# Performance work log

Measured on AMD Instinct MI355X. Metric: run time of the kernel, lower is better.

Reference implementation:

```python
import jax, jax.numpy as jnp
import numpy as np

D_MODEL = 1024
N_HEAD = 16
POWER = 4
EPS = 1e-6
MASK_FILL = -1000.0


def setup_inputs() -> dict:
    key = jax.random.key(0)
    ks = jax.random.split(key, 10)
    B, T, C = 2, 2048, D_MODEL
    sc = 1.0 / np.sqrt(C)
    inp = {
        "x": jax.random.normal(ks[0], (B, T, C), jnp.float32),
        "Wq": jax.random.normal(ks[1], (C, C), jnp.float32) * sc,
        "bq": jnp.zeros((C,), jnp.float32),
        "Wk": jax.random.normal(ks[2], (C, C), jnp.float32) * sc,
        "bk": jnp.zeros((C,), jnp.float32),
        "Wv": jax.random.normal(ks[3], (C, C), jnp.float32) * sc,
        "bv": jnp.zeros((C,), jnp.float32),
        "Wo": jax.random.normal(ks[4], (C, C), jnp.float32) * sc,
        "bo": jnp.zeros((C,), jnp.float32),
        "score_gain": jnp.asarray(4.0, jnp.float32),
        # True above the diagonal -> masked (causal)
        "causal_mask": jnp.triu(jnp.ones((T, T), jnp.bool_), k=1),
    }
    return inp


def rational_softmax(x):
    s = x / (jnp.abs(x) + 1.0)          # squash to (-1, 1)
    p = ((s + 1.0) * 0.5) ** POWER      # (0,1) then sharpen
    return p / (jnp.sum(p, axis=-1, keepdims=True) + EPS)


def reference(x, Wq, bq, Wk, bk, Wv, bv, Wo, bo, score_gain, causal_mask):
    B, T, C = x.shape
    H, D = N_HEAD, C // N_HEAD
    q = (x @ Wq + bq).reshape(B, T, H, D)
    k = (x @ Wk + bk).reshape(B, T, H, D)
    v = (x @ Wv + bv).reshape(B, T, H, D)
    # scores: (B, H, T, T)
    scores = jnp.einsum('bqhd,bkhd->bhqk', q, k)
    scores = scores - jnp.mean(scores, axis=-1, keepdims=True)
    mad = jnp.mean(jnp.abs(scores), axis=-1, keepdims=True) + 1e-6
    scores = scores / mad * score_gain
    scores = jnp.where(causal_mask, MASK_FILL, scores)
    attn = rational_softmax(scores)
    out = jnp.einsum('bhqk,bkhd->bqhd', attn, v).reshape(B, T, C)
    return out @ Wo + bo
```

## Files before the change

### kernel.cpp

```cpp
#include <hip/hip_runtime.h>
#include <hip/hip_bf16.h>
#include <cstdint>

#define BDIM 2
#define TSEQ 2048
#define CDIM 1024
#define NH 16
#define HD 64
#define NTOK (BDIM*TSEQ)
#define MASK_FILL_V (-1000.0f)
#define EPS_V (1e-6f)

typedef short bf16x8 __attribute__((ext_vector_type(8)));
typedef float f32x4  __attribute__((ext_vector_type(4)));

__device__ __forceinline__ float bf2f(unsigned short u) {
    union { unsigned int i; float f; } x; x.i = ((unsigned int)u) << 16; return x.f;
}
__device__ __forceinline__ unsigned short f2bf(float v) {
    __hip_bfloat16 h = __float2bfloat16(v);
    union { __hip_bfloat16 h; unsigned short u; } c; c.h = h; return c.u;
}
__device__ __forceinline__ float unpk_lo(unsigned int u) {
    union { unsigned int i; float f; } x; x.i = u << 16; return x.f;
}
__device__ __forceinline__ float unpk_hi(unsigned int u) {
    union { unsigned int i; float f; } x; x.i = u & 0xFFFF0000u; return x.f;
}
__device__ __forceinline__ unsigned int pk2(float lo, float hi) {
    unsigned int r;
    asm("v_cvt_pk_bf16_f32 %0, %1, %2" : "=v"(r) : "v"(lo), "v"(hi));
    return r;
}

__device__ __forceinline__ bool dt_is_bf16(const void* gain_p) {
    return ((*(const unsigned int*)gain_p) & 0xFFFFu) == 0x4080u;
}
__device__ __forceinline__ float ld1(const void* p, size_t i, bool bf) {
    return bf ? bf2f(((const unsigned short*)p)[i]) : ((const float*)p)[i];
}

__device__ __forceinline__ void gl2lds16(const unsigned short* g, unsigned short* l) {
    __builtin_amdgcn_global_load_lds(
        (const __attribute__((address_space(1))) unsigned int*)g,
        (__attribute__((address_space(3))) unsigned int*)l, 16, 0, 0);
}

__global__ __launch_bounds__(256) void pack_x_kernel(
    const void* __restrict__ X, const void* __restrict__ gain_p,
    unsigned short* __restrict__ Xb)
{
    const bool bf = dt_is_bf16(gain_p);
    size_t i = ((size_t)blockIdx.x * 256 + threadIdx.x) * 8;
    if (bf) {
        *(bf16x8*)&Xb[i] = *(const bf16x8*)((const unsigned short*)X + i);
    } else {
        const float* xf = (const float*)X;
        float4 a = *(const float4*)&xf[i];
        float4 b = *(const float4*)&xf[i + 4];
        bf16x8 o;
        o[0]=(short)f2bf(a.x); o[1]=(short)f2bf(a.y); o[2]=(short)f2bf(a.z); o[3]=(short)f2bf(a.w);
        o[4]=(short)f2bf(b.x); o[5]=(short)f2bf(b.y); o[6]=(short)f2bf(b.z); o[7]=(short)f2bf(b.w);
        *(bf16x8*)&Xb[i] = o;
    }
}

__global__ __launch_bounds__(256) void pack_wt_kernel(
    const void* __restrict__ Wq, const void* __restrict__ Wk,
    const void* __restrict__ Wv, const void* __restrict__ Wo,
    const void* __restrict__ gain_p, unsigned short* __restrict__ Wt)
{
    __shared__ __align__(16) unsigned short tile[64][72];
    const bool bf = dt_is_bf16(gain_p);
    const int which = blockIdx.z;
    const void* W = (which == 0) ? Wq : (which == 1) ? Wk : (which == 2) ? Wv : Wo;
    const int k0 = blockIdx.y * 64, n0 = blockIdx.x * 64;
    const int t = threadIdx.x;
    const int r = t >> 2, cb = (t & 3) * 16;
    if (bf) {
        const unsigned short* wsd = (const unsigned short*)W;
        *(bf16x8*)&tile[r][cb]     = *(const bf16x8*)&wsd[(size_t)(k0 + r) * CDIM + n0 + cb];
        *(bf16x8*)&tile[r][cb + 8] = *(const bf16x8*)&wsd[(size_t)(k0 + r) * CDIM + n0 + cb + 8];
    } else {
        const float* wf = (const float*)W;
        const float* src = &wf[(size_t)(k0 + r) * CDIM + n0 + cb];
        float4 f0 = *(const float4*)&src[0];
        float4 f1 = *(const float4*)&src[4];
        float4 f2 = *(const float4*)&src[8];
        float4 f3 = *(const float4*)&src[12];
        bf16x8 o0, o1;
        o0[0]=(short)f2bf(f0.x); o0[1]=(short)f2bf(f0.y); o0[2]=(short)f2bf(f0.z); o0[3]=(short)f2bf(f0.w);
        o0[4]=(short)f2bf(f1.x); o0[5]=(short)f2bf(f1.y); o0[6]=(short)f2bf(f1.z); o0[7]=(short)f2bf(f1.w);
        o1[0]=(short)f2bf(f2.x); o1[1]=(short)f2bf(f2.y); o1[2]=(short)f2bf(f2.z); o1[3]=(short)f2bf(f2.w);
        o1[4]=(short)f2bf(f3.x); o1[5]=(short)f2bf(f3.y); o1[6]=(short)f2bf(f3.z); o1[7]=(short)f2bf(f3.w);
        *(bf16x8*)&tile[r][cb]     = o0;
        *(bf16x8*)&tile[r][cb + 8] = o1;
    }
    __syncthreads();
    const int dr = t >> 2, tb = (t & 3) * 16;
    __align__(16) unsigned short tmp[16];
#pragma unroll
    for (int j = 0; j < 16; ++j) tmp[j] = tile[tb + j][dr];
    unsigned short* dst = Wt + ((size_t)(which * CDIM + n0 + dr)) * CDIM + k0 + tb;
    *(bf16x8*)&dst[0] = *(bf16x8*)&tmp[0];
    *(bf16x8*)&dst[8] = *(bf16x8*)&tmp[8];
}

__global__ __launch_bounds__(256) void gemm_mfma_kernel(
    const unsigned short* __restrict__ A,
    const unsigned short* __restrict__ Bt,
    const void* __restrict__ b0p, const void* __restrict__ b1p,
    const void* __restrict__ b2p,
    const void* __restrict__ gain_p,
    unsigned short* __restrict__ qkv,
    void* __restrict__ outp, int mode)
{
    __shared__ __align__(16) unsigned short As[128 * 32];
    __shared__ __align__(16) unsigned short Bs[128 * 32];

    const bool bf = dt_is_bf16(gain_p);
    const int t = threadIdx.x;
    const int w = t >> 6, lane = t & 63, quad = lane >> 4, l16 = lane & 15;
    const int wm = w >> 1, wn = w & 1;

    const int gx = gridDim.x, gy = gridDim.y;
    const int lin = blockIdx.y * gx + blockIdx.x;
    const int chunk = (gx * gy) >> 3;
    const int nid = (lin & 7) * chunk + (lin >> 3);
    const int n0 = (nid / gy) * 128, m0 = (nid % gy) * 128;

    const unsigned short* Ag = A  + (size_t)m0 * CDIM;
    const unsigned short* Bg = Bt + (size_t)n0 * CDIM;

    f32x4 acc[4][4];
#pragma unroll
    for (int mt = 0; mt < 4; ++mt)
#pragma unroll
        for (int nt = 0; nt < 4; ++nt)
            acc[mt][nt] = (f32x4){0.f, 0.f, 0.f, 0.f};

    for (int kt = 0; kt < CDIM / 32; ++kt) {
        const int k0 = kt * 32;
#pragma unroll
        for (int i = 0; i < 2; ++i) {
            const int chunkid = (i * 4 + w) * 64 + lane;
            const int row = chunkid >> 2, kp = (chunkid & 3) * 8;
            gl2lds16(Ag + (size_t)row * CDIM + k0 + kp, &As[(i * 4 + w) * 512]);
            gl2lds16(Bg + (size_t)row * CDIM + k0 + kp, &Bs[(i * 4 + w) * 512]);
        }
        __syncthreads();
        bf16x8 af[4], bfr[4];
#pragma unroll
        for (int mt = 0; mt < 4; ++mt)
            af[mt] = *(const bf16x8*)&As[(wm * 64 + mt * 16 + l16) * 32 + quad * 8];
#pragma unroll
        for (int nt = 0; nt < 4; ++nt)
            bfr[nt] = *(const bf16x8*)&Bs[(wn * 64 + nt * 16 + l16) * 32 + quad * 8];
#pragma unroll
        for (int mt = 0; mt < 4; ++mt)
#pragma unroll
            for (int nt = 0; nt < 4; ++nt)
                acc[mt][nt] = __builtin_amdgcn_mfma_f32_16x16x32_bf16(af[mt], bfr[nt], acc[mt][nt], 0, 0, 0);
        __syncthreads();
    }

    if (mode == 0) {
        const int which = n0 >> 10;
        if (which < 2) {
            const void* biasP = (which == 0) ? b0p : b1p;
            unsigned short* out = qkv + (size_t)which * NTOK * CDIM;
#pragma unroll
            for (int nt = 0; nt < 4; ++nt) {
                const int np = (n0 & 1023) + wn * 64 + nt * 16 + l16;
                const int h = np >> 6, d = np & 63;
                const float bias = ld1(biasP, np, bf);
#pragma unroll
                for (int mt = 0; mt < 4; ++mt)
#pragma unroll
                    for (int r = 0; r < 4; ++r) {
                        const int m = m0 + wm * 64 + mt * 16 + quad * 4 + r;
                        const int bb = m >> 11, tt = m & (TSEQ - 1);
                        out[(((size_t)(bb * NH + h)) * TSEQ + tt) * HD + d] =
                            f2bf(acc[mt][nt][r] + bias);
                    }
            }
        } else {
            unsigned short* vt = (unsigned short*)outp;
#pragma unroll
            for (int nt = 0; nt < 4; ++nt) {
                const int np = (n0 & 1023) + wn * 64 + nt * 16 + l16;
                const int h = np >> 6, d = np & 63;
                const float bias = ld1(b2p, np, bf);
#pragma unroll
                for (int mt = 0; mt < 4; ++mt) {
                    const int m = m0 + wm * 64 + mt * 16 + quad * 4;
                    const int bb = m >> 11, tt0 = m & (TSEQ - 1);
                    unsigned int lo = ((unsigned int)f2bf(acc[mt][nt][1] + bias) << 16)
                                    |  (unsigned int)f2bf(acc[mt][nt][0] + bias);
                    unsigned int hi = ((unsigned int)f2bf(acc[mt][nt][3] + bias) << 16)
                                    |  (unsigned int)f2bf(acc[mt][nt][2] + bias);
                    uint2 pk; pk.x = lo; pk.y = hi;
                    *(uint2*)&vt[((size_t)(bb * NH + h) * HD + d) * TSEQ + tt0] = pk;
                }
            }
        }
    } else {
#pragma unroll
        for (int nt = 0; nt < 4; ++nt) {
            const int np = n0 + wn * 64 + nt * 16 + l16;
            const float bias = ld1(b0p, np, bf);
#pragma unroll
            for (int mt = 0; mt < 4; ++mt)
#pragma unroll
                for (int r = 0; r < 4; ++r) {
                    const int m = m0 + wm * 64 + mt * 16 + quad * 4 + r;
                    const float v = acc[mt][nt][r] + bias;
                    if (bf) ((__hip_bfloat16*)outp)[(size_t)m * CDIM + np] = __float2bfloat16(v);
                    else    ((float*)outp)[(size_t)m * CDIM + np] = v;
                }
        }
    }
}

__global__ __launch_bounds__(256) void ksum_kernel(
    const unsigned short* __restrict__ Kb, float* __restrict__ Ksum)
{
    __shared__ float red[32][64];
    const int bh = blockIdx.x;
    const int t = threadIdx.x;
    const int d8 = (t & 7) * 8, g = t >> 3;
    const unsigned short* kp = Kb + (size_t)bh * TSEQ * HD;
    float s[8] = {};
    for (int tt = g; tt < TSEQ; tt += 32) {
        bf16x8 v = *(const bf16x8*)&kp[(size_t)tt * HD + d8];
#pragma unroll
        for (int j = 0; j < 8; ++j) s[j] += bf2f((unsigned short)v[j]);
    }
#pragma unroll
    for (int j = 0; j < 8; ++j) red[g][d8 + j] = s[j];
    __syncthreads();
    if (t < 64) {
        float tot = 0.f;
#pragma unroll
        for (int gg = 0; gg < 32; ++gg) tot += red[gg][t];
        Ksum[(size_t)bh * HD + t] = tot;
    }
}

#define QROWS 16
#define NQT (TSEQ / QROWS)

__global__ __launch_bounds__(512, 2) void attn_mfma_kernel(
    const unsigned short* __restrict__ Qb,
    const unsigned short* __restrict__ Kb,
    const unsigned short* __restrict__ Vt,
    const float* __restrict__ Ksum,
    const void* __restrict__ gain_p,
    unsigned short* __restrict__ AOb)
{
    __shared__ float smad[2][8][16];
    __shared__ float spsum[2][8][16];
    __shared__ float pvp[8][16 * 68];

    const bool bf = dt_is_bf16(gain_p);
    const float gain = ld1(gain_p, 0, bf);

    const int t    = threadIdx.x;
    const int w    = t >> 6;
    const int lane = t & 63;
    const int quad = lane >> 4;
    const int l16  = lane & 15;
    const int b4   = quad & 1, b5 = quad >> 1;

    const int id = blockIdx.x;
    const int bh = id & 31;
    const int p  = id >> 5;
    const int q0a = p * QROWS;
    const int q0b = (NQT - 1 - p) * QROWS;
    const int b  = bh >> 4, h = bh & 15;
    const size_t base = (size_t)bh * TSEQ * HD;

    bf16x8 qfA[2], qfB[2];
    qfA[0] = *(const bf16x8*)&Qb[base + (size_t)(q0a + l16) * HD + quad * 8];
    qfA[1] = *(const bf16x8*)&Qb[base + (size_t)(q0a + l16) * HD + 32 + quad * 8];
    qfB[0] = *(const bf16x8*)&Qb[base + (size_t)(q0b + l16) * HD + quad * 8];
    qfB[1] = *(const bf16x8*)&Qb[base + (size_t)(q0b + l16) * HD + 32 + quad * 8];

    const float* Ks = Ksum + (size_t)bh * HD;
    float4 kA0 = *(const float4*)&Ks[quad * 8];
    float4 kA1 = *(const float4*)&Ks[quad * 8 + 4];
    float4 kB0 = *(const float4*)&Ks[32 + quad * 8];
    float4 kB1 = *(const float4*)&Ks[32 + quad * 8 + 4];
    auto qdot = [&](const bf16x8 (&qf)[2]) -> float {
        float m;
        m  = bf2f((unsigned short)qf[0][0]) * kA0.x;
        m  = fmaf(bf2f((unsigned short)qf[0][1]), kA0.y, m);
        m  = fmaf(bf2f((unsigned short)qf[0][2]), kA0.z, m);
        m  = fmaf(bf2f((unsigned short)qf[0][3]), kA0.w, m);
        m  = fmaf(bf2f((unsigned short)qf[0][4]), kA1.x, m);
        m  = fmaf(bf2f((unsigned short)qf[0][5]), kA1.y, m);
        m  = fmaf(bf2f((unsigned short)qf[0][6]), kA1.z, m);
        m  = fmaf(bf2f((unsigned short)qf[0][7]), kA1.w, m);
        m  = fmaf(bf2f((unsigned short)qf[1][0]), kB0.x, m);
        m  = fmaf(bf2f((unsigned short)qf[1][1]), kB0.y, m);
        m  = fmaf(bf2f((unsigned short)qf[1][2]), kB0.z, m);
        m  = fmaf(bf2f((unsigned short)qf[1][3]), kB0.w, m);
        m  = fmaf(bf2f((unsigned short)qf[1][4]), kB1.x, m);
        m  = fmaf(bf2f((unsigned short)qf[1][5]), kB1.y, m);
        m  = fmaf(bf2f((unsigned short)qf[1][6]), kB1.z, m);
        m  = fmaf(bf2f((unsigned short)qf[1][7]), kB1.w, m);
        m += __shfl_xor(m, 16);
        m += __shfl_xor(m, 32);
        return m * (1.0f / TSEQ);
    };
    const float meanA = qdot(qfA);
    const float meanB = qdot(qfB);

    const unsigned short* kp = Kb + base + (size_t)(w * 16 + l16) * HD + quad * 8;
    bf16x8 kbuf[4][2];
#pragma unroll
    for (int i = 0; i < 4; ++i) {
        kbuf[i][0] = *(const bf16x8*)&kp[(size_t)i * 8192];
        kbuf[i][1] = *(const bf16x8*)&kp[(size_t)i * 8192 + 32];
    }

    unsigned int pkwA[8][2], pkwB[16][2];
    float madpA0 = 0.f, madpA1 = 0.f, madpB0 = 0.f, madpB1 = 0.f;
#pragma unroll
    for (int i = 0; i < 16; ++i) {
        bf16x8 c0 = kbuf[i & 3][0], c1 = kbuf[i & 3][1];
        if (i + 4 < 16) {
            kbuf[i & 3][0] = *(const bf16x8*)&kp[(size_t)(i + 4) * 8192];
            kbuf[i & 3][1] = *(const bf16x8*)&kp[(size_t)(i + 4) * 8192 + 32];
        }
        f32x4 z = (f32x4){0.f, 0.f, 0.f, 0.f};
        f32x4 sA0 = __builtin_amdgcn_mfma_f32_16x16x32_bf16(c0, qfA[0], z, 0, 0, 0);
        f32x4 sA1 = __builtin_amdgcn_mfma_f32_16x16x32_bf16(c1, qfA[1], z, 0, 0, 0);
        f32x4 sB0 = __builtin_amdgcn_mfma_f32_16x16x32_bf16(c0, qfB[0], z, 0, 0, 0);
        f32x4 sB1 = __builtin_amdgcn_mfma_f32_16x16x32_bf16(c1, qfB[1], z, 0, 0, 0);
        float a0 = (sA0[0] + sA1[0]) - meanA, a1 = (sA0[1] + sA1[1]) - meanA;
        float a2 = (sA0[2] + sA1[2]) - meanA, a3 = (sA0[3] + sA1[3]) - meanA;
        madpA0 += fabsf(a0) + fabsf(a1);
        madpA1 += fabsf(a2) + fabsf(a3);
        if (i < 8) {
            pkwA[i][0] = pk2(a0, a1);
            pkwA[i][1] = pk2(a2, a3);
        }
        float e0 = (sB0[0] + sB1[0]) - meanB, e1 = (sB0[1] + sB1[1]) - meanB;
        float e2 = (sB0[2] + sB1[2]) - meanB, e3 = (sB0[3] + sB1[3]) - meanB;
        madpB0 += fabsf(e0) + fabsf(e1);
        madpB1 += fabsf(e2) + fabsf(e3);
        pkwB[i][0] = pk2(e0, e1);
        pkwB[i][1] = pk2(e2, e3);
    }
    float madpA = madpA0 + madpA1;
    float madpB = madpB0 + madpB1;
    madpA += __shfl_xor(madpA, 16);
    madpA += __shfl_xor(madpA, 32);
    madpB += __shfl_xor(madpB, 16);
    madpB += __shfl_xor(madpB, 32);
    if (lane < 16) { smad[0][w][lane] = madpA; smad[1][w][lane] = madpB; }
    __syncthreads();

    float msA = 0.f, msB = 0.f;
#pragma unroll
    for (int ww = 0; ww < 8; ++ww) { msA += smad[0][ww][l16]; msB += smad[1][ww][l16]; }
    const float scaleA = gain / (msA * (1.0f / TSEQ) + 1e-6f);
    const float scaleB = gain / (msB * (1.0f / TSEQ) + 1e-6f);

    const int NTmaxA = p;
    const int NTmaxB = NQT - 1 - p;
    const int difA = NTmaxA - w;
    const int i_maxA = (difA >= 0) ? (difA >> 3) : -1;
    const int jmaxA  = (i_maxA >= 0) ? (i_maxA >> 1) : -1;
    const int difB = NTmaxB - w;
    const int i_maxB = (difB >= 0) ? (difB >> 3) : -1;
    const int jmaxB  = (i_maxB >= 0) ? (i_maxB >> 1) : -1;

    const bool kgt0 = (quad * 4 + 0) > l16;
    const bool kgt1 = (quad * 4 + 1) > l16;
    const bool kgt2 = (quad * 4 + 2) > l16;
    const bool kgt3 = (quad * 4 + 3) > l16;

    auto rsoft = [](float vv) -> float {
        float rc = __builtin_amdgcn_rcpf(fabsf(vv) + 1.0f);
        float ss = vv * rc;
        float u  = fmaf(ss, 0.5f, 0.5f);
        float u2 = u * u;
        return u2 * u2;
    };
    auto xform = [&](unsigned int plo, unsigned int phi, bool mask, float scale,
                     float& psum, unsigned int& P0, unsigned int& P1) {
        float v0 = unpk_lo(plo) * scale, v1 = unpk_hi(plo) * scale;
        float v2 = unpk_lo(phi) * scale, v3 = unpk_hi(phi) * scale;
        if (mask) {
            if (kgt0) v0 = MASK_FILL_V;
            if (kgt1) v1 = MASK_FILL_V;
            if (kgt2) v2 = MASK_FILL_V;
            if (kgt3) v3 = MASK_FILL_V;
        }
        float p0 = rsoft(v0), p1 = rsoft(v1), p2 = rsoft(v2), p3 = rsoft(v3);
        psum += (p0 + p1) + (p2 + p3);
        P0 = pk2(p0, p1);
        P1 = pk2(p2, p3);
    };
    auto exch = [&](const unsigned int (&pk0)[2], const unsigned int (&pk1)[2],
                    bool use1, bool mask0, bool mask1, float scale,
                    float& psum, unsigned int (&fru)[4]) {
        unsigned int A0, A1, B0, B1;
        xform(pk0[0], pk0[1], mask0, scale, psum, A0, A1);
        if (use1) xform(pk1[0], pk1[1], mask1, scale, psum, B0, B1);
        else { B0 = 0u; B1 = 0u; }
        unsigned int K0 = b5 ? B0 : A0, K1 = b5 ? B1 : A1;
        unsigned int T0 = b5 ? A0 : B0, T1 = b5 ? A1 : B1;
        unsigned int R0 = (unsigned int)__shfl_xor((int)T0, 32);
        unsigned int R1 = (unsigned int)__shfl_xor((int)T1, 32);
        unsigned int S0 = (b5 ^ b4) ? K0 : R0, S1 = (b5 ^ b4) ? K1 : R1;
        unsigned int U0 = (unsigned int)__shfl_xor((int)S0, 16);
        unsigned int U1 = (unsigned int)__shfl_xor((int)S1, 16);
        fru[0] = b4 ? U0 : (b5 ? R0 : K0);
        fru[1] = b4 ? U1 : (b5 ? R1 : K1);
        fru[2] = b4 ? (b5 ? K0 : R0) : U0;
        fru[3] = b4 ? (b5 ? K1 : R1) : U1;
    };

    const unsigned short* vp = Vt + ((size_t)bh * HD + l16) * TSEQ
                               + w * 16 + b5 * 128 + b4 * 8;

    float psumA = 0.f, psumB = 0.f;
    f32x4 aA0 = (f32x4){0.f,0.f,0.f,0.f}, aA1 = (f32x4){0.f,0.f,0.f,0.f};
    f32x4 aA2 = (f32x4){0.f,0.f,0.f,0.f}, aA3 = (f32x4){0.f,0.f,0.f,0.f};
    f32x4 aB0 = (f32x4){0.f,0.f,0.f,0.f}, aB1 = (f32x4){0.f,0.f,0.f,0.f};
    f32x4 aB2 = (f32x4){0.f,0.f,0.f,0.f}, aB3 = (f32x4){0.f,0.f,0.f,0.f};
#pragma unroll
    for (int j = 0; j < 8; ++j) {
        if (j <= jmaxB) {
            bf16x8 vb0 = *(const bf16x8*)&vp[j * 256 + 0 * 32768];
            bf16x8 vb1 = *(const bf16x8*)&vp[j * 256 + 1 * 32768];
            bf16x8 vb2 = *(const bf16x8*)&vp[j * 256 + 2 * 32768];
            bf16x8 vb3 = *(const bf16x8*)&vp[j * 256 + 3 * 32768];
            unsigned int fruB[4];
            exch(pkwB[2 * j], pkwB[2 * j + 1], (2 * j + 1) <= i_maxB,
                 (w + 16 * j) == NTmaxB, (w + 16 * j + 8) == NTmaxB,
                 scaleB, psumB, fruB);
            union { unsigned int u[4]; bf16x8 v; } FB;
            FB.u[0] = fruB[0]; FB.u[1] = fruB[1]; FB.u[2] = fruB[2]; FB.u[3] = fruB[3];
            aB0 = __builtin_amdgcn_mfma_f32_16x16x32_bf16(FB.v, vb0, aB0, 0, 0, 0);
            aB1 = __builtin_amdgcn_mfma_f32_16x16x32_bf16(FB.v, vb1, aB1, 0, 0, 0);
            aB2 = __builtin_amdgcn_mfma_f32_16x16x32_bf16(FB.v, vb2, aB2, 0, 0, 0);
            aB3 = __builtin_amdgcn_mfma_f32_16x16x32_bf16(FB.v, vb3, aB3, 0, 0, 0);
            if (j < 4) {
                if (j <= jmaxA) {
                    unsigned int fruA[4];
                    exch(pkwA[2 * j], pkwA[2 * j + 1], (2 * j + 1) <= i_maxA,
                         (w + 16 * j) == NTmaxA, (w + 16 * j + 8) == NTmaxA,
                         scaleA, psumA, fruA);
                    union { unsigned int u[4]; bf16x8 v; } FA;
                    FA.u[0] = fruA[0]; FA.u[1] = fruA[1]; FA.u[2] = fruA[2]; FA.u[3] = fruA[3];
                    aA0 = __builtin_amdgcn_mfma_f32_16x16x32_bf16(FA.v, vb0, aA0, 0, 0, 0);
                    aA1 = __builtin_amdgcn_mfma_f32_16x16x32_bf16(FA.v, vb1, aA1, 0, 0, 0);
                    aA2 = __builtin_amdgcn_mfma_f32_16x16x32_bf16(FA.v, vb2, aA2, 0, 0, 0);
                    aA3 = __builtin_amdgcn_mfma_f32_16x16x32_bf16(FA.v, vb3, aA3, 0, 0, 0);
                }
            }
        }
    }

    psumA += __shfl_xor(psumA, 16);
    psumA += __shfl_xor(psumA, 32);
    psumB += __shfl_xor(psumB, 16);
    psumB += __shfl_xor(psumB, 32);
    if (lane < 16) { spsum[0][w][lane] = psumA; spsum[1][w][lane] = psumB; }

#pragma unroll
    for (int r = 0; r < 4; ++r) {
        const int qi = quad * 4 + r;
        pvp[w][qi * 68 +      l16] = aA0[r];
        pvp[w][qi * 68 + 16 + l16] = aA1[r];
        pvp[w][qi * 68 + 32 + l16] = aA2[r];
        pvp[w][qi * 68 + 48 + l16] = aA3[r];
    }
    __syncthreads();
    {
        const int q  = t >> 5;
        const int d2 = (t & 31) * 2;
        float s0 = 0.f, s1 = 0.f;
#pragma unroll
        for (int ww = 0; ww < 8; ++ww) {
            const float* pp = &pvp[ww][q * 68 + d2];
            s0 += pp[0];
            s1 += pp[1];
        }
        float ps = 0.f;
#pragma unroll
        for (int ww = 0; ww < 8; ++ww) ps += spsum[0][ww][q];
        const float inv = 1.0f / (ps + EPS_V);
        unsigned int o = ((unsigned int)f2bf(s1 * inv) << 16) | (unsigned int)f2bf(s0 * inv);
        *(unsigned int*)&AOb[((size_t)(b * TSEQ + q0a + q)) * CDIM + h * HD + d2] = o;
    }
    __syncthreads();

#pragma unroll
    for (int r = 0; r < 4; ++r) {
        const int qi = quad * 4 + r;
        pvp[w][qi * 68 +      l16] = aB0[r];
        pvp[w][qi * 68 + 16 + l16] = aB1[r];
        pvp[w][qi * 68 + 32 + l16] = aB2[r];
        pvp[w][qi * 68 + 48 + l16] = aB3[r];
    }
    __syncthreads();
    {
        const int q  = t >> 5;
        const int d2 = (t & 31) * 2;
        float s0 = 0.f, s1 = 0.f;
#pragma unroll
        for (int ww = 0; ww < 8; ++ww) {
            const float* pp = &pvp[ww][q * 68 + d2];
            s0 += pp[0];
            s1 += pp[1];
        }
        float ps = 0.f;
#pragma unroll
        for (int ww = 0; ww < 8; ++ww) ps += spsum[1][ww][q];
        const float inv = 1.0f / (ps + EPS_V);
        unsigned int o = ((unsigned int)f2bf(s1 * inv) << 16) | (unsigned int)f2bf(s0 * inv);
        *(unsigned int*)&AOb[((size_t)(b * TSEQ + q0b + q)) * CDIM + h * HD + d2] = o;
    }
}

extern "C" void kernel_launch(void* const* d_in, const int* in_sizes, int n_in,
                              void* d_out, int out_size, void* d_ws, size_t ws_size,
                              hipStream_t stream)
{
    (void)in_sizes; (void)n_in; (void)out_size; (void)ws_size;
    const void* X    = d_in[0];
    const void* Wq   = d_in[1];
    const void* bq   = d_in[2];
    const void* Wk   = d_in[3];
    const void* bk   = d_in[4];
    const void* Wv   = d_in[5];
    const void* bv   = d_in[6];
    const void* Wo   = d_in[7];
    const void* bo   = d_in[8];
    const void* gain = d_in[9];

    char* ws = (char*)d_ws;
    unsigned short* Xb  = (unsigned short*)ws;
    unsigned short* Wt  = (unsigned short*)(ws + (8ull  << 20));
    unsigned short* QKV = (unsigned short*)(ws + (16ull << 20));
    unsigned short* Vt  = (unsigned short*)(ws + (40ull << 20));
    unsigned short* AOb = (unsigned short*)(ws + (48ull << 20));
    float*          Ks  = (float*)(ws + (56ull << 20));
    unsigned short* Qb  = QKV;
    unsigned short* Kb  = QKV + (size_t)NTOK * CDIM;

    pack_x_kernel<<<NTOK * CDIM / (256 * 8), 256, 0, stream>>>(X, gain, Xb);
    pack_wt_kernel<<<dim3(16, 16, 4), 256, 0, stream>>>(Wq, Wk, Wv, Wo, gain, Wt);

    dim3 g1(3 * CDIM / 128, NTOK / 128);
    gemm_mfma_kernel<<<g1, 256, 0, stream>>>(Xb, Wt, bq, bk, bv, gain, QKV, Vt, 0);

    ksum_kernel<<<BDIM * NH, 256, 0, stream>>>(Kb, Ks);

    attn_mfma_kernel<<<(NQT / 2) * BDIM * NH, 512, 0, stream>>>(
        Qb, Kb, Vt, Ks, gain, AOb);

    dim3 g3(CDIM / 128, NTOK / 128);
    gemm_mfma_kernel<<<g3, 256, 0, stream>>>(AOb, Wt + 3ull * CDIM * CDIM, bo, bo, bo, gain,
                                             nullptr, d_out, 1);
}
```

Baseline: 312.3 us.

## Fuse K column-sum into QKV GEMM epilogue and stage V transpose through LDS

```diff
diff --git a/kernel.cpp b/kernel.cpp
--- a/kernel.cpp
+++ b/kernel.cpp
@@ -48,9 +48,13 @@
 
 __global__ __launch_bounds__(256) void pack_x_kernel(
     const void* __restrict__ X, const void* __restrict__ gain_p,
-    unsigned short* __restrict__ Xb)
+    unsigned short* __restrict__ Xb, float* __restrict__ Ks)
 {
     const bool bf = dt_is_bf16(gain_p);
+    if (blockIdx.x == 0) {
+#pragma unroll
+        for (int k = 0; k < 8; ++k) Ks[threadIdx.x * 8 + k] = 0.f;
+    }
     size_t i = ((size_t)blockIdx.x * 256 + threadIdx.x) * 8;
     if (bf) {
         *(bf16x8*)&Xb[i] = *(const bf16x8*)((const unsigned short*)X + i);
@@ -113,10 +117,11 @@
     const void* __restrict__ b2p,
     const void* __restrict__ gain_p,
     unsigned short* __restrict__ qkv,
-    void* __restrict__ outp, int mode)
+    void* __restrict__ outp, float* __restrict__ Ksum, int mode)
 {
     __shared__ __align__(16) unsigned short As[128 * 32];
     __shared__ __align__(16) unsigned short Bs[128 * 32];
+    __shared__ __align__(16) unsigned short vstage[128][66];
 
     const bool bf = dt_is_bf16(gain_p);
     const int t = threadIdx.x;
@@ -166,6 +171,8 @@
 
     if (mode == 0) {
         const int which = n0 >> 10;
+        const int bb = m0 >> 11;
+        const int mloc = m0 & (TSEQ - 1);
         if (which < 2) {
             const void* biasP = (which == 0) ? b0p : b1p;
             unsigned short* out = qkv + (size_t)which * NTOK * CDIM;
@@ -174,34 +181,54 @@
                 const int np = (n0 & 1023) + wn * 64 + nt * 16 + l16;
                 const int h = np >> 6, d = np & 63;
                 const float bias = ld1(biasP, np, bf);
+                float sum16 = 0.f;
 #pragma unroll
                 for (int mt = 0; mt < 4; ++mt)
 #pragma unroll
                     for (int r = 0; r < 4; ++r) {
                         const int m = m0 + wm * 64 + mt * 16 + quad * 4 + r;
-                        const int bb = m >> 11, tt = m & (TSEQ - 1);
-                        out[(((size_t)(bb * NH + h)) * TSEQ + tt) * HD + d] =
-                            f2bf(acc[mt][nt][r] + bias);
+                        const int tt = m & (TSEQ - 1);
+                        unsigned short us = f2bf(acc[mt][nt][r] + bias);
+                        out[(((size_t)(bb * NH + h)) * TSEQ + tt) * HD + d] = us;
+                        sum16 += bf2f(us);
                     }
+                if (which == 1)
+                    atomicAdd(&Ksum[((size_t)(bb * NH + h)) * HD + d], sum16);
             }
         } else {
             unsigned short* vt = (unsigned short*)outp;
 #pragma unroll
-            for (int nt = 0; nt < 4; ++nt) {
-                const int np = (n0 & 1023) + wn * 64 + nt * 16 + l16;
-                const int h = np >> 6, d = np & 63;
-                const float bias = ld1(b2p, np, bf);
-#pragma unroll
-                for (int mt = 0; mt < 4; ++mt) {
-                    const int m = m0 + wm * 64 + mt * 16 + quad * 4;
-                    const int bb = m >> 11, tt0 = m & (TSEQ - 1);
-                    unsigned int lo = ((unsigned int)f2bf(acc[mt][nt][1] + bias) << 16)
-                                    |  (unsigned int)f2bf(acc[mt][nt][0] + bias);
-                    unsigned int hi = ((unsigned int)f2bf(acc[mt][nt][3] + bias) << 16)
-                                    |  (unsigned int)f2bf(acc[mt][nt][2] + bias);
-                    uint2 pk; pk.x = lo; pk.y = hi;
-                    *(uint2*)&vt[((size_t)(bb * NH + h) * HD + d) * TSEQ + tt0] = pk;
+            for (int half = 0; half < 2; ++half) {
+                if (wn == half) {
+#pragma unroll
+                    for (int nt = 0; nt < 4; ++nt) {
+                        const int np = (n0 & 1023) + wn * 64 + nt * 16 + l16;
+                        const float bias = ld1(b2p, np, bf);
+                        const int nl = nt * 16 + l16;
+#pragma unroll
+                        for (int mt = 0; mt < 4; ++mt)
+#pragma unroll
+                            for (int r = 0; r < 4; ++r) {
+                                const int tl = wm * 64 + mt * 16 + quad * 4 + r;
+                                vstage[tl][nl] = f2bf(acc[mt][nt][r] + bias);
+                            }
+                    }
                 }
+                __syncthreads();
+#pragma unroll
+                for (int c = 0; c < 4; ++c) {
+                    const int ck = t + 256 * c;
+                    const int nl = ck >> 4;
+                    const int tb = (ck & 15) * 8;
+                    const int np = (n0 & 1023) + half * 64 + nl;
+                    const int h = np >> 6, d = np & 63;
+                    __align__(16) unsigned short tmp[8];
+#pragma unroll
+                    for (int k = 0; k < 8; ++k) tmp[k] = vstage[tb + k][nl];
+                    *(bf16x8*)&vt[((size_t)(bb * NH + h) * HD + d) * TSEQ + mloc + tb] =
+                        *(bf16x8*)tmp;
+                }
+                __syncthreads();
             }
         }
     } else {
@@ -219,31 +246,6 @@
                     else    ((float*)outp)[(size_t)m * CDIM + np] = v;
                 }
         }
-    }
-}
-
-__global__ __launch_bounds__(256) void ksum_kernel(
-    const unsigned short* __restrict__ Kb, float* __restrict__ Ksum)
-{
-    __shared__ float red[32][64];
-    const int bh = blockIdx.x;
-    const int t = threadIdx.x;
-    const int d8 = (t & 7) * 8, g = t >> 3;
-    const unsigned short* kp = Kb + (size_t)bh * TSEQ * HD;
-    float s[8] = {};
-    for (int tt = g; tt < TSEQ; tt += 32) {
-        bf16x8 v = *(const bf16x8*)&kp[(size_t)tt * HD + d8];
-#pragma unroll
-        for (int j = 0; j < 8; ++j) s[j] += bf2f((unsigned short)v[j]);
-    }
-#pragma unroll
-    for (int j = 0; j < 8; ++j) red[g][d8 + j] = s[j];
-    __syncthreads();
-    if (t < 64) {
-        float tot = 0.f;
-#pragma unroll
-        for (int gg = 0; gg < 32; ++gg) tot += red[gg][t];
-        Ksum[(size_t)bh * HD + t] = tot;
     }
 }
 
@@ -554,18 +556,16 @@
     unsigned short* Qb  = QKV;
     unsigned short* Kb  = QKV + (size_t)NTOK * CDIM;
 
-    pack_x_kernel<<<NTOK * CDIM / (256 * 8), 256, 0, stream>>>(X, gain, Xb);
+    pack_x_kernel<<<NTOK * CDIM / (256 * 8), 256, 0, stream>>>(X, gain, Xb, Ks);
     pack_wt_kernel<<<dim3(16, 16, 4), 256, 0, stream>>>(Wq, Wk, Wv, Wo, gain, Wt);
 
     dim3 g1(3 * CDIM / 128, NTOK / 128);
-    gemm_mfma_kernel<<<g1, 256, 0, stream>>>(Xb, Wt, bq, bk, bv, gain, QKV, Vt, 0);
-
-    ksum_kernel<<<BDIM * NH, 256, 0, stream>>>(Kb, Ks);
+    gemm_mfma_kernel<<<g1, 256, 0, stream>>>(Xb, Wt, bq, bk, bv, gain, QKV, Vt, Ks, 0);
 
     attn_mfma_kernel<<<(NQT / 2) * BDIM * NH, 512, 0, stream>>>(
         Qb, Kb, Vt, Ks, gain, AOb);
 
     dim3 g3(CDIM / 128, NTOK / 128);
     gemm_mfma_kernel<<<g3, 256, 0, stream>>>(AOb, Wt + 3ull * CDIM * CDIM, bo, bo, bo, gain,
-                                             nullptr, d_out, 1);
-}
+                                             nullptr, d_out, nullptr, 1);
+}
```

Result: slower. 319.8 us (+2.4%).
